# Kernel tuning notes

Hardware: AMD Instinct MI355X
Metric: run time of the kernel (lower is better)

## Reference

```python
import jax, jax.numpy as jnp
import numpy as np

NUM_SPLITS = 64
UNITS_PER_SPLIT = 64
IN_DIM = 4096          # divisible by NUM_SPLITS -> 64 input features per split
OUT_DIM = NUM_SPLITS * UNITS_PER_SPLIT  # 4096
BATCH = 4096
BN_EPS = 1e-3          # keras BatchNormalization default epsilon


def make_mask():
    # block_diag of NUM_SPLITS ones-blocks of shape (IN_DIM//NUM_SPLITS, UNITS_PER_SPLIT)
    din_per = IN_DIM // NUM_SPLITS
    return jnp.kron(jnp.eye(NUM_SPLITS, dtype=jnp.float32),
                    jnp.ones((din_per, UNITS_PER_SPLIT), dtype=jnp.float32))


def setup_inputs() -> dict:
    key = jax.random.key(0)
    k_x, k_w = jax.random.split(key)
    x = jax.random.normal(k_x, (BATCH, IN_DIM), dtype=jnp.float32)
    weight = jax.random.normal(k_w, (IN_DIM, OUT_DIM), dtype=jnp.float32) * (2.0 / IN_DIM) ** 0.5
    bias = jnp.full((OUT_DIM,), 0.1, dtype=jnp.float32)
    gamma = jnp.ones((OUT_DIM,), dtype=jnp.float32)
    beta = jnp.zeros((OUT_DIM,), dtype=jnp.float32)
    return {"x": x, "weight": weight, "bias": bias, "gamma": gamma, "beta": beta}


def reference(x, weight, bias, gamma, beta):
    mask = make_mask()  # [IN_DIM, OUT_DIM] block-diagonal 0/1
    # masked dense: only block-diagonal entries of weight participate
    out = jnp.matmul(x, weight * mask) + bias  # [B, OUT_DIM]
    # BatchNorm, training=True: batch statistics (biased variance), keras eps=1e-3
    mean = jnp.mean(out, axis=0)
    var = jnp.mean(jnp.square(out - mean), axis=0)
    out = (out - mean) * jax.lax.rsqrt(var + BN_EPS) * gamma + beta
    return jax.nn.relu(out)
```

## Files before the change

### kernel.cpp

```cpp
#include <hip/hip_runtime.h>

#define BATCH 4096
#define DIM 4096
#define NSPLIT 64
#define ROWS_PB 128
#define NCHUNK 32
#define BN_EPS 1e-3f

typedef __attribute__((ext_vector_type(8))) short bf16x8;
typedef __attribute__((ext_vector_type(8))) unsigned short ushort8;
typedef __attribute__((ext_vector_type(4))) float f32x4;

__device__ inline unsigned short f2bf(float f) {
    union { float f; unsigned int u; } c; c.f = f;
    unsigned int u = c.u;
    u += 0x7FFFu + ((u >> 16) & 1u);
    return (unsigned short)(u >> 16);
}

__device__ inline float bf2f(unsigned short h) {
    union { unsigned int u; float f; } c;
    c.u = (unsigned int)h << 16;
    return c.f;
}

__global__ __launch_bounds__(256) void gemm_stats(
    const float* __restrict__ x, const float* __restrict__ w,
    float* __restrict__ part, float* __restrict__ out)
{
    __shared__ unsigned short wt[64][72];
    __shared__ float red1[4][64], red2[4][64];

    const int s  = blockIdx.y;
    const int r0 = blockIdx.x * ROWS_PB;
    const int t  = threadIdx.x;
    const int lane = t & 63, wave = t >> 6;
    const int quad = lane >> 4, l16 = lane & 15;

    for (int i = t; i < 1024; i += 256) {
        int k = i >> 4, c4 = i & 15;
        float4 v = *(const float4*)(w + (size_t)(s*64 + k) * DIM + s*64 + c4*4);
        wt[c4*4 + 0][k] = f2bf(v.x);
        wt[c4*4 + 1][k] = f2bf(v.y);
        wt[c4*4 + 2][k] = f2bf(v.z);
        wt[c4*4 + 3][k] = f2bf(v.w);
    }

    float4 xv[2][2][2];
    #pragma unroll
    for (int rt = 0; rt < 2; rt++)
        #pragma unroll
        for (int kk = 0; kk < 2; kk++)
            #pragma unroll
            for (int h = 0; h < 2; h++)
                xv[rt][kk][h] = *(const float4*)(
                    x + (size_t)(r0 + wave*32 + rt*16 + l16) * DIM
                      + s*64 + kk*32 + quad*8 + h*4);

    __syncthreads();

    bf16x8 af[2][2], bfr[4][2];
    #pragma unroll
    for (int rt = 0; rt < 2; rt++)
        #pragma unroll
        for (int kk = 0; kk < 2; kk++) {
            bf16x8 a;
            a[0] = (short)f2bf(xv[rt][kk][0].x);
            a[1] = (short)f2bf(xv[rt][kk][0].y);
            a[2] = (short)f2bf(xv[rt][kk][0].z);
            a[3] = (short)f2bf(xv[rt][kk][0].w);
            a[4] = (short)f2bf(xv[rt][kk][1].x);
            a[5] = (short)f2bf(xv[rt][kk][1].y);
            a[6] = (short)f2bf(xv[rt][kk][1].z);
            a[7] = (short)f2bf(xv[rt][kk][1].w);
            af[rt][kk] = a;
        }
    #pragma unroll
    for (int ct = 0; ct < 4; ct++)
        #pragma unroll
        for (int kk = 0; kk < 2; kk++)
            bfr[ct][kk] = *(const bf16x8*)&wt[ct*16 + l16][kk*32 + quad*8];

    f32x4 acc[2][4];
    #pragma unroll
    for (int rt = 0; rt < 2; rt++)
        #pragma unroll
        for (int ct = 0; ct < 4; ct++)
            acc[rt][ct] = (f32x4){0.f, 0.f, 0.f, 0.f};

    #pragma unroll
    for (int kk = 0; kk < 2; kk++)
        #pragma unroll
        for (int rt = 0; rt < 2; rt++)
            #pragma unroll
            for (int ct = 0; ct < 4; ct++)
                acc[rt][ct] = __builtin_amdgcn_mfma_f32_16x16x32_bf16(
                    af[rt][kk], bfr[ct][kk], acc[rt][ct], 0, 0, 0);

    #pragma unroll
    for (int j = 0; j < 4; j++) {
        const int f0 = 2*j, f1 = 2*j + 1;
        const f32x4 a0 = acc[f0 >> 2][f0 & 3];
        const f32x4 a1 = acc[f1 >> 2][f1 & 3];
        ushort8 pk;
        pk[0] = f2bf(a0[0]); pk[1] = f2bf(a0[1]);
        pk[2] = f2bf(a0[2]); pk[3] = f2bf(a0[3]);
        pk[4] = f2bf(a1[0]); pk[5] = f2bf(a1[1]);
        pk[6] = f2bf(a1[2]); pk[7] = f2bf(a1[3]);
        int u = j*256 + t;
        unsigned short* dst =
            (unsigned short*)(out + (size_t)(r0 + (u >> 4)) * DIM + s*64)
            + (u & 15) * 8;
        *(ushort8*)dst = pk;
    }

    float s1[4], s2[4];
    #pragma unroll
    for (int ct = 0; ct < 4; ct++) { s1[ct] = 0.f; s2[ct] = 0.f; }
    #pragma unroll
    for (int rt = 0; rt < 2; rt++)
        #pragma unroll
        for (int ct = 0; ct < 4; ct++)
            #pragma unroll
            for (int r = 0; r < 4; r++) {
                float v = acc[rt][ct][r];
                s1[ct] += v; s2[ct] += v * v;
            }
    #pragma unroll
    for (int ct = 0; ct < 4; ct++) {
        float a = s1[ct], b = s2[ct];
        a += __shfl_xor(a, 16); b += __shfl_xor(b, 16);
        a += __shfl_xor(a, 32); b += __shfl_xor(b, 32);
        if (quad == 0) {
            red1[wave][ct*16 + l16] = a;
            red2[wave][ct*16 + l16] = b;
        }
    }
    __syncthreads();
    if (t < 64) {
        float a = red1[0][t] + red1[1][t] + red1[2][t] + red1[3][t];
        float b = red2[0][t] + red2[1][t] + red2[2][t] + red2[3][t];
        size_t base = (size_t)(s * NCHUNK + blockIdx.x) * 128;
        part[base + t]      = a;
        part[base + 64 + t] = b;
    }
}

__global__ __launch_bounds__(256) void bn_apply(
    const float* __restrict__ part, const float* __restrict__ gamma,
    const float* __restrict__ beta, float* __restrict__ out)
{
    __shared__ float redA[4][64], redB[4][64];
    __shared__ float scol[64], shcol[64];

    const int s  = blockIdx.y;
    const int r0 = blockIdx.x * ROWS_PB;
    const int t  = threadIdx.x;
    const int lane = t & 63, wave = t >> 6;
    const int quad = lane >> 4, l16 = lane & 15;

    ushort8 yv[4];
    #pragma unroll
    for (int j = 0; j < 4; j++) {
        int u = j*256 + t;
        const unsigned short* src =
            (const unsigned short*)(out + (size_t)(r0 + (u >> 4)) * DIM + s*64)
            + (u & 15) * 8;
        yv[j] = *(const ushort8*)src;
    }

    {
        float a = 0.f, b = 0.f;
        #pragma unroll
        for (int p8 = 0; p8 < 8; p8++) {
            int p = wave*8 + p8;
            size_t base = (size_t)(s * NCHUNK + p) * 128;
            a += part[base + lane];
            b += part[base + 64 + lane];
        }
        redA[wave][lane] = a;
        redB[wave][lane] = b;
    }

    asm volatile("s_waitcnt vmcnt(0)" ::: "memory");
    __syncthreads();

    if (t < 64) {
        float a = redA[0][t] + redA[1][t] + redA[2][t] + redA[3][t];
        float b = redB[0][t] + redB[1][t] + redB[2][t] + redB[3][t];
        float mean = a * (1.f / BATCH);
        float var  = b * (1.f / BATCH) - mean * mean;
        float rstd = rsqrtf(var + BN_EPS);
        float sc = gamma[s*64 + t] * rstd;
        scol[t]  = sc;
        shcol[t] = beta[s*64 + t] - mean * sc;
    }
    __syncthreads();

    #pragma unroll
    for (int j = 0; j < 4; j++) {
        #pragma unroll
        for (int h = 0; h < 2; h++) {
            const int f  = 2*j + h;
            const int rt = f >> 2, ct = f & 3;
            const int col = ct*16 + l16;
            const float sc = scol[col], sh = shcol[col];
            #pragma unroll
            for (int r = 0; r < 4; r++) {
                float v = fmaxf(fmaf(bf2f((unsigned short)yv[j][h*4 + r]), sc, sh), 0.f);
                int row = r0 + wave*32 + rt*16 + quad*4 + r;
                out[(size_t)row * DIM + s*64 + col] = v;
            }
        }
    }
}

extern "C" void kernel_launch(void* const* d_in, const int* in_sizes, int n_in,
                              void* d_out, int out_size, void* d_ws, size_t ws_size,
                              hipStream_t stream) {
    const float* x     = (const float*)d_in[0];
    const float* w     = (const float*)d_in[1];
    const float* gamma = (const float*)d_in[3];
    const float* beta  = (const float*)d_in[4];
    float* out  = (float*)d_out;
    float* part = (float*)d_ws;

    gemm_stats<<<dim3(NCHUNK, NSPLIT), 256, 0, stream>>>(x, w, part, out);
    bn_apply<<<dim3(NCHUNK, NSPLIT), 256, 0, stream>>>(part, gamma, beta, out);
}
```

Measured before the change: 177.5 us.

## Process four row chunks per GEMM block with double-buffered x loads

Each gemm_stats block now handles four 128-row chunks instead of one. The weight tile is converted once and reused across those chunks, and the x loads for the next chunk are prefetched into a second register buffer while the current chunk is computed. The partial-statistics layout shrinks from 32 to 8 entries per split, and bn_apply reduces fewer partials. The grid drops to 512 blocks, which cuts redundant weight staging and partial traffic but lowers parallelism and raises register pressure.

```diff
diff --git a/kernel.cpp b/kernel.cpp
--- a/kernel.cpp
+++ b/kernel.cpp
@@ -5,6 +5,8 @@
 #define NSPLIT 64
 #define ROWS_PB 128
 #define NCHUNK 32
+#define CPB 4
+#define BLKX 8
 #define BN_EPS 1e-3f
 
 typedef __attribute__((ext_vector_type(8))) short bf16x8;
@@ -32,7 +34,7 @@
     __shared__ float red1[4][64], red2[4][64];
 
     const int s  = blockIdx.y;
-    const int r0 = blockIdx.x * ROWS_PB;
+    const int c0 = blockIdx.x * CPB;
     const int t  = threadIdx.x;
     const int lane = t & 63, wave = t >> 6;
     const int quad = lane >> 4, l16 = lane & 15;
@@ -46,86 +48,103 @@
         wt[c4*4 + 3][k] = f2bf(v.w);
     }
 
-    float4 xv[2][2][2];
-    #pragma unroll
-    for (int rt = 0; rt < 2; rt++)
-        #pragma unroll
-        for (int kk = 0; kk < 2; kk++)
-            #pragma unroll
-            for (int h = 0; h < 2; h++)
-                xv[rt][kk][h] = *(const float4*)(
-                    x + (size_t)(r0 + wave*32 + rt*16 + l16) * DIM
-                      + s*64 + kk*32 + quad*8 + h*4);
-
-    __syncthreads();
-
-    bf16x8 af[2][2], bfr[4][2];
-    #pragma unroll
-    for (int rt = 0; rt < 2; rt++)
-        #pragma unroll
-        for (int kk = 0; kk < 2; kk++) {
-            bf16x8 a;
-            a[0] = (short)f2bf(xv[rt][kk][0].x);
-            a[1] = (short)f2bf(xv[rt][kk][0].y);
-            a[2] = (short)f2bf(xv[rt][kk][0].z);
-            a[3] = (short)f2bf(xv[rt][kk][0].w);
-            a[4] = (short)f2bf(xv[rt][kk][1].x);
-            a[5] = (short)f2bf(xv[rt][kk][1].y);
-            a[6] = (short)f2bf(xv[rt][kk][1].z);
-            a[7] = (short)f2bf(xv[rt][kk][1].w);
-            af[rt][kk] = a;
-        }
+    auto load_chunk = [&](float4 (&dst)[2][2][2], int c) {
+        const int rr0 = (c0 + c) * ROWS_PB;
+        #pragma unroll
+        for (int rt = 0; rt < 2; rt++)
+            #pragma unroll
+            for (int kk = 0; kk < 2; kk++)
+                #pragma unroll
+                for (int h = 0; h < 2; h++)
+                    dst[rt][kk][h] = *(const float4*)(
+                        x + (size_t)(rr0 + wave*32 + rt*16 + l16) * DIM
+                          + s*64 + kk*32 + quad*8 + h*4);
+    };
+
+    float4 xvA[2][2][2], xvB[2][2][2];
+    load_chunk(xvA, 0);
+
+    __syncthreads();
+
+    bf16x8 bfr[4][2];
     #pragma unroll
     for (int ct = 0; ct < 4; ct++)
         #pragma unroll
         for (int kk = 0; kk < 2; kk++)
             bfr[ct][kk] = *(const bf16x8*)&wt[ct*16 + l16][kk*32 + quad*8];
 
-    f32x4 acc[2][4];
-    #pragma unroll
-    for (int rt = 0; rt < 2; rt++)
-        #pragma unroll
-        for (int ct = 0; ct < 4; ct++)
-            acc[rt][ct] = (f32x4){0.f, 0.f, 0.f, 0.f};
-
-    #pragma unroll
-    for (int kk = 0; kk < 2; kk++)
+    float s1[4], s2[4];
+    #pragma unroll
+    for (int ct = 0; ct < 4; ct++) { s1[ct] = 0.f; s2[ct] = 0.f; }
+
+    #pragma unroll
+    for (int c = 0; c < CPB; c++) {
+        float4 (&cur)[2][2][2] = (c & 1) ? xvB : xvA;
+        float4 (&nxt)[2][2][2] = (c & 1) ? xvA : xvB;
+        if (c < CPB - 1) load_chunk(nxt, c + 1);
+
+        bf16x8 af[2][2];
+        #pragma unroll
+        for (int rt = 0; rt < 2; rt++)
+            #pragma unroll
+            for (int kk = 0; kk < 2; kk++) {
+                bf16x8 a;
+                a[0] = (short)f2bf(cur[rt][kk][0].x);
+                a[1] = (short)f2bf(cur[rt][kk][0].y);
+                a[2] = (short)f2bf(cur[rt][kk][0].z);
+                a[3] = (short)f2bf(cur[rt][kk][0].w);
+                a[4] = (short)f2bf(cur[rt][kk][1].x);
+                a[5] = (short)f2bf(cur[rt][kk][1].y);
+                a[6] = (short)f2bf(cur[rt][kk][1].z);
+                a[7] = (short)f2bf(cur[rt][kk][1].w);
+                af[rt][kk] = a;
+            }
+
+        f32x4 acc[2][4];
         #pragma unroll
         for (int rt = 0; rt < 2; rt++)
             #pragma unroll
             for (int ct = 0; ct < 4; ct++)
-                acc[rt][ct] = __builtin_amdgcn_mfma_f32_16x16x32_bf16(
-                    af[rt][kk], bfr[ct][kk], acc[rt][ct], 0, 0, 0);
-
-    #pragma unroll
-    for (int j = 0; j < 4; j++) {
-        const int f0 = 2*j, f1 = 2*j + 1;
-        const f32x4 a0 = acc[f0 >> 2][f0 & 3];
-        const f32x4 a1 = acc[f1 >> 2][f1 & 3];
-        ushort8 pk;
-        pk[0] = f2bf(a0[0]); pk[1] = f2bf(a0[1]);
-        pk[2] = f2bf(a0[2]); pk[3] = f2bf(a0[3]);
-        pk[4] = f2bf(a1[0]); pk[5] = f2bf(a1[1]);
-        pk[6] = f2bf(a1[2]); pk[7] = f2bf(a1[3]);
-        int u = j*256 + t;
-        unsigned short* dst =
-            (unsigned short*)(out + (size_t)(r0 + (u >> 4)) * DIM + s*64)
-            + (u & 15) * 8;
-        *(ushort8*)dst = pk;
-    }
-
-    float s1[4], s2[4];
-    #pragma unroll
-    for (int ct = 0; ct < 4; ct++) { s1[ct] = 0.f; s2[ct] = 0.f; }
-    #pragma unroll
-    for (int rt = 0; rt < 2; rt++)
-        #pragma unroll
-        for (int ct = 0; ct < 4; ct++)
-            #pragma unroll
-            for (int r = 0; r < 4; r++) {
-                float v = acc[rt][ct][r];
-                s1[ct] += v; s2[ct] += v * v;
-            }
+                acc[rt][ct] = (f32x4){0.f, 0.f, 0.f, 0.f};
+
+        #pragma unroll
+        for (int kk = 0; kk < 2; kk++)
+            #pragma unroll
+            for (int rt = 0; rt < 2; rt++)
+                #pragma unroll
+                for (int ct = 0; ct < 4; ct++)
+                    acc[rt][ct] = __builtin_amdgcn_mfma_f32_16x16x32_bf16(
+                        af[rt][kk], bfr[ct][kk], acc[rt][ct], 0, 0, 0);
+
+        const int rr0 = (c0 + c) * ROWS_PB;
+        #pragma unroll
+        for (int j = 0; j < 4; j++) {
+            const int f0 = 2*j, f1 = 2*j + 1;
+            const f32x4 a0 = acc[f0 >> 2][f0 & 3];
+            const f32x4 a1 = acc[f1 >> 2][f1 & 3];
+            ushort8 pk;
+            pk[0] = f2bf(a0[0]); pk[1] = f2bf(a0[1]);
+            pk[2] = f2bf(a0[2]); pk[3] = f2bf(a0[3]);
+            pk[4] = f2bf(a1[0]); pk[5] = f2bf(a1[1]);
+            pk[6] = f2bf(a1[2]); pk[7] = f2bf(a1[3]);
+            int u = j*256 + t;
+            unsigned short* dst =
+                (unsigned short*)(out + (size_t)(rr0 + (u >> 4)) * DIM + s*64)
+                + (u & 15) * 8;
+            *(ushort8*)dst = pk;
+        }
+
+        #pragma unroll
+        for (int rt = 0; rt < 2; rt++)
+            #pragma unroll
+            for (int ct = 0; ct < 4; ct++)
+                #pragma unroll
+                for (int r = 0; r < 4; r++) {
+                    float v = acc[rt][ct][r];
+                    s1[ct] += v; s2[ct] += v * v;
+                }
+    }
+
     #pragma unroll
     for (int ct = 0; ct < 4; ct++) {
         float a = s1[ct], b = s2[ct];
@@ -140,7 +159,7 @@
     if (t < 64) {
         float a = red1[0][t] + red1[1][t] + red1[2][t] + red1[3][t];
         float b = red2[0][t] + red2[1][t] + red2[2][t] + red2[3][t];
-        size_t base = (size_t)(s * NCHUNK + blockIdx.x) * 128;
+        size_t base = (size_t)(s * BLKX + blockIdx.x) * 128;
         part[base + t]      = a;
         part[base + 64 + t] = b;
     }
@@ -172,9 +191,9 @@
     {
         float a = 0.f, b = 0.f;
         #pragma unroll
-        for (int p8 = 0; p8 < 8; p8++) {
-            int p = wave*8 + p8;
-            size_t base = (size_t)(s * NCHUNK + p) * 128;
+        for (int p2 = 0; p2 < 2; p2++) {
+            int p = wave*2 + p2;
+            size_t base = (size_t)(s * BLKX + p) * 128;
             a += part[base + lane];
             b += part[base + 64 + lane];
         }
@@ -225,6 +244,6 @@
     float* out  = (float*)d_out;
     float* part = (float*)d_ws;
 
-    gemm_stats<<<dim3(NCHUNK, NSPLIT), 256, 0, stream>>>(x, w, part, out);
+    gemm_stats<<<dim3(BLKX, NSPLIT), 256, 0, stream>>>(x, w, part, out);
     bn_apply<<<dim3(NCHUNK, NSPLIT), 256, 0, stream>>>(part, gamma, beta, out);
 }
```

After: 180.1 us. Within noise of the previous version (+1.5%).

## Stage x rows for four splits in LDS with coalesced loads in gemm kernel

Applied to the files above, without the earlier changes.

Each gemm block now covers four splits (256 contiguous input columns) using 512 threads. It loads x rows with fully coalesced float4 reads into a bf16 LDS tile instead of scattered per-lane 64-column reads, and each wave pair computes 64 rows of one split. The bf16 output mapping changes, so bn_apply's decode loop is updated to match. The aim is better global-load efficiency and fewer, larger blocks, at the cost of more LDS per block and fewer blocks in the grid.

```diff
diff --git a/kernel.cpp b/kernel.cpp
--- a/kernel.cpp
+++ b/kernel.cpp
@@ -5,7 +5,10 @@
 #define NSPLIT 64
 #define ROWS_PB 128
 #define NCHUNK 32
+#define SPB 4
+#define SGRP 16
 #define BN_EPS 1e-3f
+#define XS_LD 264
 
 typedef __attribute__((ext_vector_type(8))) short bf16x8;
 typedef __attribute__((ext_vector_type(8))) unsigned short ushort8;
@@ -24,66 +27,61 @@
     return c.f;
 }
 
-__global__ __launch_bounds__(256) void gemm_stats(
+__global__ __launch_bounds__(512) void gemm_stats(
     const float* __restrict__ x, const float* __restrict__ w,
     float* __restrict__ part, float* __restrict__ out)
 {
-    __shared__ unsigned short wt[64][72];
-    __shared__ float red1[4][64], red2[4][64];
-
-    const int s  = blockIdx.y;
+    __shared__ unsigned short xs[ROWS_PB][XS_LD];
+    __shared__ unsigned short wt[SPB][64][72];
+    __shared__ float red1[8][64], red2[8][64];
+
+    const int sg = blockIdx.y;
     const int r0 = blockIdx.x * ROWS_PB;
     const int t  = threadIdx.x;
     const int lane = t & 63, wave = t >> 6;
     const int quad = lane >> 4, l16 = lane & 15;
-
-    for (int i = t; i < 1024; i += 256) {
-        int k = i >> 4, c4 = i & 15;
-        float4 v = *(const float4*)(w + (size_t)(s*64 + k) * DIM + s*64 + c4*4);
-        wt[c4*4 + 0][k] = f2bf(v.x);
-        wt[c4*4 + 1][k] = f2bf(v.y);
-        wt[c4*4 + 2][k] = f2bf(v.z);
-        wt[c4*4 + 3][k] = f2bf(v.w);
-    }
-
-    float4 xv[2][2][2];
-    #pragma unroll
-    for (int rt = 0; rt < 2; rt++)
+    const int sp = wave >> 1;
+    const int hw = wave & 1;
+    const int s  = sg * SPB + sp;
+
+    #pragma unroll
+    for (int it = 0; it < 16; it++) {
+        int i = t + it * 512;
+        int row = i >> 6, c4 = i & 63;
+        float4 v = *(const float4*)(x + (size_t)(r0 + row) * DIM + sg*256 + c4*4);
+        ushort4 u;
+        u.x = f2bf(v.x); u.y = f2bf(v.y); u.z = f2bf(v.z); u.w = f2bf(v.w);
+        *(ushort4*)&xs[row][c4*4] = u;
+    }
+
+    #pragma unroll
+    for (int it = 0; it < 8; it++) {
+        int i = t + it * 512;
+        int spw = i >> 10, k = (i >> 4) & 63, c4 = i & 15;
+        int sw = sg * SPB + spw;
+        float4 v = *(const float4*)(w + (size_t)(sw*64 + k) * DIM + sw*64 + c4*4);
+        wt[spw][c4*4 + 0][k] = f2bf(v.x);
+        wt[spw][c4*4 + 1][k] = f2bf(v.y);
+        wt[spw][c4*4 + 2][k] = f2bf(v.z);
+        wt[spw][c4*4 + 3][k] = f2bf(v.w);
+    }
+    __syncthreads();
+
+    bf16x8 af[4][2], bfr[4][2];
+    #pragma unroll
+    for (int rt = 0; rt < 4; rt++)
         #pragma unroll
         for (int kk = 0; kk < 2; kk++)
-            #pragma unroll
-            for (int h = 0; h < 2; h++)
-                xv[rt][kk][h] = *(const float4*)(
-                    x + (size_t)(r0 + wave*32 + rt*16 + l16) * DIM
-                      + s*64 + kk*32 + quad*8 + h*4);
-
-    __syncthreads();
-
-    bf16x8 af[2][2], bfr[4][2];
-    #pragma unroll
-    for (int rt = 0; rt < 2; rt++)
-        #pragma unroll
-        for (int kk = 0; kk < 2; kk++) {
-            bf16x8 a;
-            a[0] = (short)f2bf(xv[rt][kk][0].x);
-            a[1] = (short)f2bf(xv[rt][kk][0].y);
-            a[2] = (short)f2bf(xv[rt][kk][0].z);
-            a[3] = (short)f2bf(xv[rt][kk][0].w);
-            a[4] = (short)f2bf(xv[rt][kk][1].x);
-            a[5] = (short)f2bf(xv[rt][kk][1].y);
-            a[6] = (short)f2bf(xv[rt][kk][1].z);
-            a[7] = (short)f2bf(xv[rt][kk][1].w);
-            af[rt][kk] = a;
-        }
+            af[rt][kk] = *(const bf16x8*)&xs[hw*64 + rt*16 + l16][sp*64 + kk*32 + quad*8];
     #pragma unroll
     for (int ct = 0; ct < 4; ct++)
         #pragma unroll
         for (int kk = 0; kk < 2; kk++)
-            bfr[ct][kk] = *(const bf16x8*)&wt[ct*16 + l16][kk*32 + quad*8];
-
-    f32x4 acc[2][4];
-    #pragma unroll
-    for (int rt = 0; rt < 2; rt++)
+            bfr[ct][kk] = *(const bf16x8*)&wt[sp][ct*16 + l16][kk*32 + quad*8];
+
+    f32x4 acc[4][4];
+    #pragma unroll
+    for (int rt = 0; rt < 4; rt++)
         #pragma unroll
         for (int ct = 0; ct < 4; ct++)
             acc[rt][ct] = (f32x4){0.f, 0.f, 0.f, 0.f};
@@ -91,34 +89,35 @@
     #pragma unroll
     for (int kk = 0; kk < 2; kk++)
         #pragma unroll
-        for (int rt = 0; rt < 2; rt++)
+        for (int rt = 0; rt < 4; rt++)
             #pragma unroll
             for (int ct = 0; ct < 4; ct++)
                 acc[rt][ct] = __builtin_amdgcn_mfma_f32_16x16x32_bf16(
                     af[rt][kk], bfr[ct][kk], acc[rt][ct], 0, 0, 0);
 
     #pragma unroll
-    for (int j = 0; j < 4; j++) {
-        const int f0 = 2*j, f1 = 2*j + 1;
-        const f32x4 a0 = acc[f0 >> 2][f0 & 3];
-        const f32x4 a1 = acc[f1 >> 2][f1 & 3];
-        ushort8 pk;
-        pk[0] = f2bf(a0[0]); pk[1] = f2bf(a0[1]);
-        pk[2] = f2bf(a0[2]); pk[3] = f2bf(a0[3]);
-        pk[4] = f2bf(a1[0]); pk[5] = f2bf(a1[1]);
-        pk[6] = f2bf(a1[2]); pk[7] = f2bf(a1[3]);
-        int u = j*256 + t;
-        unsigned short* dst =
-            (unsigned short*)(out + (size_t)(r0 + (u >> 4)) * DIM + s*64)
-            + (u & 15) * 8;
-        *(ushort8*)dst = pk;
-    }
+    for (int rt = 0; rt < 4; rt++)
+        #pragma unroll
+        for (int jp = 0; jp < 2; jp++) {
+            const f32x4 a0 = acc[rt][jp*2 + 0];
+            const f32x4 a1 = acc[rt][jp*2 + 1];
+            ushort8 pk;
+            pk[0] = f2bf(a0[0]); pk[1] = f2bf(a0[1]);
+            pk[2] = f2bf(a0[2]); pk[3] = f2bf(a0[3]);
+            pk[4] = f2bf(a1[0]); pk[5] = f2bf(a1[1]);
+            pk[6] = f2bf(a1[2]); pk[7] = f2bf(a1[3]);
+            int u = (rt*2 + jp)*128 + hw*64 + lane;
+            unsigned short* dst =
+                (unsigned short*)(out + (size_t)(r0 + (u >> 4)) * DIM + s*64)
+                + (u & 15) * 8;
+            *(ushort8*)dst = pk;
+        }
 
     float s1[4], s2[4];
     #pragma unroll
     for (int ct = 0; ct < 4; ct++) { s1[ct] = 0.f; s2[ct] = 0.f; }
     #pragma unroll
-    for (int rt = 0; rt < 2; rt++)
+    for (int rt = 0; rt < 4; rt++)
         #pragma unroll
         for (int ct = 0; ct < 4; ct++)
             #pragma unroll
@@ -137,12 +136,14 @@
         }
     }
     __syncthreads();
-    if (t < 64) {
-        float a = red1[0][t] + red1[1][t] + red1[2][t] + red1[3][t];
-        float b = red2[0][t] + red2[1][t] + red2[2][t] + red2[3][t];
-        size_t base = (size_t)(s * NCHUNK + blockIdx.x) * 128;
-        part[base + t]      = a;
-        part[base + 64 + t] = b;
+
+    if (t < 256) {
+        int sp2 = t >> 6, col = t & 63;
+        float a = red1[sp2*2 + 0][col] + red1[sp2*2 + 1][col];
+        float b = red2[sp2*2 + 0][col] + red2[sp2*2 + 1][col];
+        size_t base = (size_t)((sg*SPB + sp2) * NCHUNK + blockIdx.x) * 128;
+        part[base + col]      = a;
+        part[base + 64 + col] = b;
     }
 }
 
@@ -157,16 +158,15 @@
     const int r0 = blockIdx.x * ROWS_PB;
     const int t  = threadIdx.x;
     const int lane = t & 63, wave = t >> 6;
-    const int quad = lane >> 4, l16 = lane & 15;
 
     ushort8 yv[4];
     #pragma unroll
-    for (int j = 0; j < 4; j++) {
-        int u = j*256 + t;
+    for (int jj = 0; jj < 4; jj++) {
+        int u = jj*256 + t;
         const unsigned short* src =
             (const unsigned short*)(out + (size_t)(r0 + (u >> 4)) * DIM + s*64)
             + (u & 15) * 8;
-        yv[j] = *(const ushort8*)src;
+        yv[jj] = *(const ushort8*)src;
     }
 
     {
@@ -198,19 +198,23 @@
     __syncthreads();
 
     #pragma unroll
-    for (int j = 0; j < 4; j++) {
-        #pragma unroll
-        for (int h = 0; h < 2; h++) {
-            const int f  = 2*j + h;
-            const int rt = f >> 2, ct = f & 3;
-            const int col = ct*16 + l16;
-            const float sc = scol[col], sh = shcol[col];
-            #pragma unroll
-            for (int r = 0; r < 4; r++) {
-                float v = fmaxf(fmaf(bf2f((unsigned short)yv[j][h*4 + r]), sc, sh), 0.f);
-                int row = r0 + wave*32 + rt*16 + quad*4 + r;
-                out[(size_t)row * DIM + s*64 + col] = v;
-            }
+    for (int jj = 0; jj < 4; jj++) {
+        int u   = jj*256 + t;
+        int idx = u >> 7;
+        int tt  = u & 127;
+        int hw  = tt >> 6;
+        int ln  = tt & 63;
+        int qd  = ln >> 4, lw = ln & 15;
+        int rt  = idx >> 1, jp = idx & 1;
+        #pragma unroll
+        for (int k = 0; k < 8; k++) {
+            int ct  = jp*2 + (k >> 2);
+            int r   = k & 3;
+            int row = r0 + hw*64 + rt*16 + qd*4 + r;
+            int col = ct*16 + lw;
+            float v = fmaxf(fmaf(bf2f((unsigned short)yv[jj][k]),
+                                 scol[col], shcol[col]), 0.f);
+            out[(size_t)row * DIM + s*64 + col] = v;
         }
     }
 }
@@ -225,6 +229,6 @@
     float* out  = (float*)d_out;
     float* part = (float*)d_ws;
 
-    gemm_stats<<<dim3(NCHUNK, NSPLIT), 256, 0, stream>>>(x, w, part, out);
+    gemm_stats<<<dim3(NCHUNK, SGRP), 512, 0, stream>>>(x, w, part, out);
     bn_apply<<<dim3(NCHUNK, NSPLIT), 256, 0, stream>>>(part, gamma, beta, out);
 }
```

Result: no change. 180.6 us (+1.7%).
